# Kernel optimization log

Hardware: AMD Instinct MI355X
Metric: run time of the kernel (lower is better)

Reference implementation:

```python
import jax, jax.numpy as jnp
import numpy as np
import math

N_NODES = 50000
N_EDGES = 1600000
C = 256
H = 8
HD = C // H


def setup_inputs() -> dict:
    key = jax.random.key(0)
    ks = jax.random.split(key, 16)
    s = 0.02
    d = {
        "feat": jax.random.normal(ks[0], (N_NODES, C), jnp.float32),
        "edge_src": jax.random.randint(ks[1], (N_EDGES,), 0, N_NODES),
        "edge_dst": jax.random.randint(ks[2], (N_EDGES,), 0, N_NODES),
        # torch nn.Linear weights are [out, in]
        "Wq": jax.random.normal(ks[3], (C, C), jnp.float32) * s,
        "bq": jnp.zeros((C,), jnp.float32),
        "Wk": jax.random.normal(ks[4], (C, C), jnp.float32) * s,
        "bk": jnp.zeros((C,), jnp.float32),
        "Wv": jax.random.normal(ks[5], (C, C), jnp.float32) * s,
        "bv": jnp.zeros((C,), jnp.float32),
        "Wp": jax.random.normal(ks[6], (C, C), jnp.float32) * s,
        "bp": jnp.zeros((C,), jnp.float32),
        "ln_g": jnp.ones((C,), jnp.float32),
        "ln_b": jnp.zeros((C,), jnp.float32),
        "W1": jax.random.normal(ks[7], (4 * C, C), jnp.float32) * s,
        "b1": jnp.zeros((4 * C,), jnp.float32),
        "W2": jax.random.normal(ks[8], (C, 4 * C), jnp.float32) * s,
        "b2": jnp.zeros((C,), jnp.float32),
    }
    return d


def _layernorm(x, g, b, eps=1e-5):
    mu = jnp.mean(x, axis=-1, keepdims=True)
    var = jnp.mean(jnp.square(x - mu), axis=-1, keepdims=True)
    return (x - mu) * jax.lax.rsqrt(var + eps) * g + b


def reference(feat, edge_src, edge_dst, Wq, bq, Wk, bk, Wv, bv, Wp, bp,
              ln_g, ln_b, W1, b1, W2, b2):
    n = feat.shape[0]
    q = (feat @ Wq.T + bq).reshape(n, H, HD)
    k = (feat @ Wk.T + bk).reshape(n, H, HD)
    v = (feat @ Wv.T + bv).reshape(n, H, HD)

    # per-edge attention logits: (q[dst] * k[src]).sum(-1) / sqrt(head_dim), clamped
    score = jnp.einsum('ehd,ehd->eh', q[edge_dst], k[edge_src])  # [E, H]
    score = jnp.clip(score / math.sqrt(HD), -10.0, 10.0)

    # destination-grouped (segment) softmax over incoming edges
    smax = jax.ops.segment_max(score, edge_dst, num_segments=n)
    smax = jnp.where(jnp.isfinite(smax), smax, 0.0)  # guard empty segments
    ex = jnp.exp(score - smax[edge_dst])
    den = jax.ops.segment_sum(ex, edge_dst, num_segments=n)
    alpha = ex / den[edge_dst]  # [E, H]

    # weighted scatter-aggregate: sum_e alpha_e * v[src_e] into dst
    wv = jax.ops.segment_sum(alpha[:, :, None] * v[edge_src], edge_dst,
                             num_segments=n).reshape(n, C)

    y = wv @ Wp.T + bp
    x = feat + y
    h = _layernorm(x, ln_g, ln_b)
    h = jax.nn.gelu(h @ W1.T + b1, approximate=False) @ W2.T + b2
    return x + h
```

## Files before the change

### kernel.cpp

```cpp
#include <hip/hip_runtime.h>
#include <hip/hip_bf16.h>

#define CDIM 256
#define NH 8
#define HDIM 32

typedef short bf8 __attribute__((ext_vector_type(8)));
typedef float f32x4 __attribute__((ext_vector_type(4)));
typedef float f32x2 __attribute__((ext_vector_type(2)));

__device__ __forceinline__ float bf2f(ushort u) {
  union { unsigned int i; float f; } x; x.i = ((unsigned int)u) << 16; return x.f;
}
__device__ __forceinline__ ushort f2bf(float f) {
  union { float f; unsigned int i; } x; x.f = f;
  unsigned int lsb = (x.i >> 16) & 1u;
  unsigned int r = x.i + 0x7fffu + lsb;
  return (ushort)(r >> 16);
}

__device__ __forceinline__ float dec_e4m3_sw(unsigned int b) {
  unsigned int s = b >> 7, e = (b >> 3) & 15, m = b & 7;
  float v = (e == 0) ? (float)m * 0.001953125f
                     : (float)(8 + m) * 0.125f * exp2f((float)((int)e - 7));
  return s ? -v : v;
}
__device__ __forceinline__ unsigned char enc_e4m3_sw(float f) {
  union { float f; unsigned int u; } x; x.f = f;
  unsigned int s = (x.u >> 31) << 7;
  float a = fabsf(f);
  if (!(a > 0.f)) return (unsigned char)s;
  if (a > 448.f) a = 448.f;
  int e = 0; float mant = frexpf(a, &e);
  int E = e + 6;
  unsigned int out;
  if (E <= 0) {
    int m = (int)rintf(a * 512.f);
    out = (m > 7) ? (s | (1u << 3)) : (s | (unsigned)m);
  } else {
    int m = (int)rintf(mant * 16.f);
    if (m == 16) { m = 8; E++; }
    if (E > 15 || (E == 15 && m - 8 > 6)) { E = 15; m = 14; }
    out = s | ((unsigned)E << 3) | (unsigned)(m - 8);
  }
  return (unsigned char)out;
}
template <bool HI>
__device__ __forceinline__ f32x2 fp8x2_f32(unsigned int w) {
#if __has_builtin(__builtin_amdgcn_cvt_pk_f32_fp8)
  return __builtin_amdgcn_cvt_pk_f32_fp8(w, HI);
#else
  unsigned int b0 = HI ? ((w >> 16) & 0xffu) : (w & 0xffu);
  unsigned int b1 = HI ? (w >> 24) : ((w >> 8) & 0xffu);
  f32x2 r; r[0] = dec_e4m3_sw(b0); r[1] = dec_e4m3_sw(b1); return r;
#endif
}
__device__ __forceinline__ unsigned char f32_fp8(float f) {
#if __has_builtin(__builtin_amdgcn_cvt_pk_fp8_f32)
  return (unsigned char)(__builtin_amdgcn_cvt_pk_fp8_f32(f, f, 0, false) & 0xff);
#else
  return enc_e4m3_sw(f);
#endif
}

__device__ __forceinline__ float fast_gelu(float t) {
  float u = 0.7978845608028654f * (t + 0.044715f * t * t * t);
  float ez = __expf(2.f * u);
  float th = 1.f - 2.f * __builtin_amdgcn_rcpf(ez + 1.f);
  return 0.5f * t * (1.f + th);
}

__device__ __forceinline__ void gload_lds16(const ushort* g, ushort* l) {
  __builtin_amdgcn_global_load_lds((const __attribute__((address_space(1))) unsigned int*)g,
                                   (__attribute__((address_space(3))) unsigned int*)l,
                                   16, 0, 0);
}

__global__ void k_cast4(const float4* __restrict__ s, ushort4* __restrict__ d, int n4) {
  int i = blockIdx.x * blockDim.x + threadIdx.x;
  if (i < n4) {
    float4 v = s[i];
    ushort4 o;
    o.x = f2bf(v.x); o.y = f2bf(v.y); o.z = f2bf(v.z); o.w = f2bf(v.w);
    d[i] = o;
  }
}

__global__ void k_castw(const float4* __restrict__ s0, ushort4* __restrict__ d0,
                        const float4* __restrict__ s1, ushort4* __restrict__ d1,
                        const float4* __restrict__ s2, ushort4* __restrict__ d2,
                        const float4* __restrict__ s3, ushort4* __restrict__ d3,
                        const float4* __restrict__ s4, ushort4* __restrict__ d4,
                        const float4* __restrict__ s5, ushort4* __restrict__ d5) {
  int y = blockIdx.y;
  const float4* s; ushort4* d; int n4;
  switch (y) {
    case 0: s = s0; d = d0; n4 = 16384; break;
    case 1: s = s1; d = d1; n4 = 16384; break;
    case 2: s = s2; d = d2; n4 = 16384; break;
    case 3: s = s3; d = d3; n4 = 16384; break;
    case 4: s = s4; d = d4; n4 = 65536; break;
    default: s = s5; d = d5; n4 = 65536; break;
  }
  int i = blockIdx.x * blockDim.x + threadIdx.x;
  if (i < n4) {
    float4 v = s[i];
    ushort4 o;
    o.x = f2bf(v.x); o.y = f2bf(v.y); o.z = f2bf(v.z); o.w = f2bf(v.w);
    d[i] = o;
  }
}

__global__ void k_hist(const int* __restrict__ dst, int E, int* __restrict__ deg) {
  int i = blockIdx.x * blockDim.x + threadIdx.x;
  if (i < E) atomicAdd(&deg[dst[i]], 1);
}

__global__ __launch_bounds__(1024) void k_scan1(const int* __restrict__ deg, int N,
                                                int* __restrict__ rowptr, int* __restrict__ bsum) {
  __shared__ int s[1024];
  int t = threadIdx.x;
  int i = blockIdx.x * 1024 + t;
  int val = (i < N) ? deg[i] : 0;
  s[t] = val;
  __syncthreads();
  for (int off = 1; off < 1024; off <<= 1) {
    int add = (t >= off) ? s[t - off] : 0;
    __syncthreads();
    s[t] += add;
    __syncthreads();
  }
  if (i < N) rowptr[i + 1] = s[t];
  if (t == 1023) bsum[blockIdx.x] = s[t];
}

__global__ void k_scan2(int* __restrict__ bsum, int nb) {
  if (threadIdx.x == 0 && blockIdx.x == 0) {
    int run = 0;
    for (int j = 0; j < nb; ++j) { int t = bsum[j]; bsum[j] = run; run += t; }
  }
}

__global__ void k_scan3(int* __restrict__ rowptr, const int* __restrict__ bsum, int N) {
  int i = blockIdx.x * blockDim.x + threadIdx.x;
  if (i < N) rowptr[i + 1] += bsum[i >> 10];
  if (i == 0) rowptr[0] = 0;
}

__global__ void k_scatter(const int* __restrict__ src, const int* __restrict__ dst, int E,
                          const int* __restrict__ rowptr, int* __restrict__ cur,
                          int* __restrict__ csr_src) {
  int i = blockIdx.x * blockDim.x + threadIdx.x;
  if (i < E) {
    int d = dst[i];
    int pos = rowptr[d] + atomicAdd(&cur[d], 1);
    csr_src[pos] = src[i];
  }
}

__device__ __forceinline__ void stageA8(const ushort* __restrict__ S, int ld,
                                        int r0, int nr, int k0,
                                        ushort* lds, int wave, int lane) {
  int g = wave * 64 + lane;
  int row = g >> 2, slot = g & 3;
  int rr = r0 + row; rr = (rr < nr) ? rr : (nr - 1);
  const ushort* src = S + (size_t)rr * ld + k0 + ((slot ^ (row & 3)) << 3);
  gload_lds16(src, &lds[(size_t)(wave * 64) * 8]);
}

__device__ __forceinline__ void stageB8(const ushort* __restrict__ S, int ld,
                                        int r0, int nr, int k0,
                                        ushort* lds, int wave, int lane) {
#pragma unroll
  for (int j = 0; j < 2; ++j) {
    int g = wave * 128 + j * 64 + lane;
    int row = g >> 2, slot = g & 3;
    int rr = r0 + row; rr = (rr < nr) ? rr : (nr - 1);
    const ushort* src = S + (size_t)rr * ld + k0 + ((slot ^ (row & 3)) << 3);
    gload_lds16(src, &lds[(size_t)(wave * 128 + j * 64) * 8]);
  }
}

__device__ __forceinline__ void gemm256_core(const ushort* __restrict__ A, int lda, int rowt, int nA,
                                             const ushort* __restrict__ B, int ldb, int colt, int nB,
                                             int K, ushort* lA, ushort* lB, f32x4* acc) {
  int tid = threadIdx.x;
  int wave = tid >> 6, lane = tid & 63;
  int m = lane & 15, quad = lane >> 4;
  int r0w = (wave & 1) * 64, c0w = (wave >> 1) * 64;
  int sw = (quad ^ (m & 3)) << 3;

  for (int k0 = 0; k0 < K; k0 += 32) {
    __syncthreads();
    stageA8(A, lda, rowt, nA, k0, lA, wave, lane);
    stageB8(B, ldb, colt, nB, k0, lB, wave, lane);
    __syncthreads();

    bf8 a[4], b[4];
#pragma unroll
    for (int ri = 0; ri < 4; ++ri)
      a[ri] = *(const bf8*)&lA[(r0w + ri * 16 + m) * 32 + sw];
#pragma unroll
    for (int cj = 0; cj < 4; ++cj)
      b[cj] = *(const bf8*)&lB[(c0w + cj * 16 + m) * 32 + sw];
#pragma unroll
    for (int ri = 0; ri < 4; ++ri)
#pragma unroll
      for (int cj = 0; cj < 4; ++cj)
        acc[ri * 4 + cj] = __builtin_amdgcn_mfma_f32_16x16x32_bf16(a[ri], b[cj], acc[ri * 4 + cj], 0, 0, 0);
  }
}

__global__ __launch_bounds__(512) void k_qkvf(const ushort* __restrict__ featb,
                                              const ushort* __restrict__ Wqkv,
                                              const float* __restrict__ bq, const float* __restrict__ bk,
                                              const float* __restrict__ bv,
                                              ushort* __restrict__ q,
                                              unsigned char* __restrict__ k8,
                                              unsigned char* __restrict__ v8, int N) {
  __shared__ ushort lA[128 * 32];
  __shared__ ushort lB[256 * 32];
  int rowt = blockIdx.x * 128;
  int which = blockIdx.y;
  const float* bias = (which == 0) ? bq : (which == 1) ? bk : bv;
  int tid = threadIdx.x;
  int wave = tid >> 6, lane = tid & 63, m = lane & 15, quad = lane >> 4;
  int r0w = (wave & 1) * 64, c0w = (wave >> 1) * 64;

  f32x4 acc[16];
#pragma unroll
  for (int j = 0; j < 16; ++j) acc[j] = (f32x4){0.f, 0.f, 0.f, 0.f};

  gemm256_core(featb, CDIM, rowt, N, Wqkv + (size_t)which * 256 * CDIM, CDIM, 0, 256,
               CDIM, lA, lB, acc);

  unsigned char* o8 = (which == 1) ? k8 : v8;
#pragma unroll
  for (int cj = 0; cj < 4; ++cj) {
    int col = c0w + cj * 16 + m;
    float bs = bias[col];
#pragma unroll
    for (int ri = 0; ri < 4; ++ri)
#pragma unroll
      for (int i = 0; i < 4; ++i) {
        int r = rowt + r0w + ri * 16 + quad * 4 + i;
        if (r < N) {
          float vv = acc[ri * 4 + cj][i] + bs;
          if (which == 0) q[(size_t)r * CDIM + col] = f2bf(vv);
          else            o8[(size_t)r * CDIM + col] = f32_fp8(vv);
        }
      }
  }
}

__global__ __launch_bounds__(512) void k_projln(const ushort* __restrict__ wv,
                                                const ushort* __restrict__ Wp,
                                                const float* __restrict__ bp,
                                                const float* __restrict__ feat,
                                                const float* __restrict__ lng,
                                                const float* __restrict__ lnb,
                                                float* __restrict__ out,
                                                ushort* __restrict__ h, int N) {
  __shared__ ushort lA[128 * 32];
  __shared__ ushort lB[256 * 32];
  __shared__ float sred[2][128][4];
  int rowt = blockIdx.x * 128;
  int tid = threadIdx.x;
  int wave = tid >> 6, lane = tid & 63, m = lane & 15, quad = lane >> 4;
  int r0w = (wave & 1) * 64, c0w = (wave >> 1) * 64;

  f32x4 acc[16];
#pragma unroll
  for (int j = 0; j < 16; ++j) acc[j] = (f32x4){0.f, 0.f, 0.f, 0.f};

  gemm256_core(wv, CDIM, rowt, N, Wp, CDIM, 0, 256, CDIM, lA, lB, acc);

#pragma unroll
  for (int cj = 0; cj < 4; ++cj) {
    int col = c0w + cj * 16 + m;
    float bs = bp[col];
#pragma unroll
    for (int ri = 0; ri < 4; ++ri)
#pragma unroll
      for (int i = 0; i < 4; ++i) {
        int r = rowt + r0w + ri * 16 + quad * 4 + i;
        int rr = (r < N) ? r : (N - 1);
        acc[ri * 4 + cj][i] += bs + feat[(size_t)rr * CDIM + col];
      }
  }

#pragma unroll
  for (int ri = 0; ri < 4; ++ri)
#pragma unroll
    for (int i = 0; i < 4; ++i) {
      float s = acc[ri * 4 + 0][i] + acc[ri * 4 + 1][i] + acc[ri * 4 + 2][i] + acc[ri * 4 + 3][i];
      float ss = acc[ri * 4 + 0][i] * acc[ri * 4 + 0][i] + acc[ri * 4 + 1][i] * acc[ri * 4 + 1][i]
               + acc[ri * 4 + 2][i] * acc[ri * 4 + 2][i] + acc[ri * 4 + 3][i] * acc[ri * 4 + 3][i];
#pragma unroll
      for (int msk = 1; msk <= 8; msk <<= 1) {
        s += __shfl_xor(s, msk);
        ss += __shfl_xor(ss, msk);
      }
      if (m == 0) {
        int blrow = (wave & 1) * 64 + ri * 16 + quad * 4 + i;
        sred[0][blrow][wave >> 1] = s;
        sred[1][blrow][wave >> 1] = ss;
      }
    }
  __syncthreads();

  float mu_[16], rs_[16];
#pragma unroll
  for (int ri = 0; ri < 4; ++ri)
#pragma unroll
    for (int i = 0; i < 4; ++i) {
      int blrow = (wave & 1) * 64 + ri * 16 + quad * 4 + i;
      float S = sred[0][blrow][0] + sred[0][blrow][1] + sred[0][blrow][2] + sred[0][blrow][3];
      float SS = sred[1][blrow][0] + sred[1][blrow][1] + sred[1][blrow][2] + sred[1][blrow][3];
      float mu = S * (1.f / CDIM);
      float var = SS * (1.f / CDIM) - mu * mu;
      mu_[ri * 4 + i] = mu;
      rs_[ri * 4 + i] = rsqrtf(var + 1e-5f);
    }

#pragma unroll
  for (int cj = 0; cj < 4; ++cj) {
    int col = c0w + cj * 16 + m;
    float gc = lng[col], bc = lnb[col];
#pragma unroll
    for (int ri = 0; ri < 4; ++ri)
#pragma unroll
      for (int i = 0; i < 4; ++i) {
        int r = rowt + r0w + ri * 16 + quad * 4 + i;
        if (r < N) {
          float v = acc[ri * 4 + cj][i];
          out[(size_t)r * CDIM + col] = v;
          h[(size_t)r * CDIM + col] = f2bf((v - mu_[ri * 4 + i]) * rs_[ri * 4 + i] * gc + bc);
        }
      }
  }
}

__global__ __launch_bounds__(512) void k_g1(const ushort* __restrict__ h,
                                            const ushort* __restrict__ W1c,
                                            const float* __restrict__ b1c,
                                            ushort* __restrict__ hid, int N) {
  __shared__ ushort lA[128 * 32];
  __shared__ ushort lB[256 * 32];
  int rowt = blockIdx.x * 128, colt = blockIdx.y * 256;
  int tid = threadIdx.x;
  int wave = tid >> 6, lane = tid & 63, m = lane & 15, quad = lane >> 4;
  int r0w = (wave & 1) * 64, c0w = (wave >> 1) * 64;

  f32x4 acc[16];
#pragma unroll
  for (int j = 0; j < 16; ++j) acc[j] = (f32x4){0.f, 0.f, 0.f, 0.f};

  gemm256_core(h, CDIM, rowt, N, W1c, CDIM, colt, 512, CDIM, lA, lB, acc);

#pragma unroll
  for (int cj = 0; cj < 4; ++cj) {
    int col = colt + c0w + cj * 16 + m;
    float bs = b1c[col];
#pragma unroll
    for (int ri = 0; ri < 4; ++ri)
#pragma unroll
      for (int i = 0; i < 4; ++i) {
        int r = rowt + r0w + ri * 16 + quad * 4 + i;
        if (r < N) hid[(size_t)r * 512 + col] = f2bf(fast_gelu(acc[ri * 4 + cj][i] + bs));
      }
  }
}

__global__ __launch_bounds__(512) void k_g2(const ushort* __restrict__ hid,
                                            const ushort* __restrict__ W2c,
                                            const float* __restrict__ b2,
                                            float* __restrict__ out, int N, int first) {
  __shared__ ushort lA[128 * 32];
  __shared__ ushort lB[256 * 32];
  int rowt = blockIdx.x * 128;
  int tid = threadIdx.x;
  int wave = tid >> 6, lane = tid & 63, m = lane & 15, quad = lane >> 4;
  int r0w = (wave & 1) * 64, c0w = (wave >> 1) * 64;

  f32x4 acc[16];
#pragma unroll
  for (int j = 0; j < 16; ++j) acc[j] = (f32x4){0.f, 0.f, 0.f, 0.f};

  gemm256_core(hid, 512, rowt, N, W2c, 1024, 0, 256, 512, lA, lB, acc);

#pragma unroll
  for (int cj = 0; cj < 4; ++cj) {
    int col = c0w + cj * 16 + m;
    float bs = first ? b2[col] : 0.f;
#pragma unroll
    for (int ri = 0; ri < 4; ++ri)
#pragma unroll
      for (int i = 0; i < 4; ++i) {
        int r = rowt + r0w + ri * 16 + quad * 4 + i;
        if (r < N) {
          size_t idx = (size_t)r * CDIM + col;
          out[idx] = out[idx] + acc[ri * 4 + cj][i] + bs;
        }
      }
  }
}

__global__ __launch_bounds__(256) void k_edge_agg(const ushort* __restrict__ q,
                                                  const unsigned char* __restrict__ kk8,
                                                  const unsigned char* __restrict__ vv8,
                                                  const int* __restrict__ rowptr,
                                                  const int* __restrict__ csr_src,
                                                  int N,
                                                  ushort* __restrict__ wv) {
  int wave = threadIdx.x >> 6, lane = threadIdx.x & 63;
  int n = blockIdx.x * 4 + wave;
  if (n >= N) return;

  int el = lane >> 3, h = lane & 7;
  int beg = rowptr[n], end = rowptr[n + 1];
  int deg = end - beg;

  float qf[32];
  {
    const ushort* qp = q + (size_t)n * CDIM + h * HDIM;
#pragma unroll
    for (int g = 0; g < 4; ++g) {
      bf8 qv = *(const bf8*)(qp + g * 8);
#pragma unroll
      for (int j = 0; j < 8; ++j) qf[g * 8 + j] = bf2f((ushort)qv[j]);
    }
  }

  float accv[4] = {0.f, 0.f, 0.f, 0.f};
  float den_part = 0.f;

  int src_n = (el < deg) ? csr_src[beg + el] : 0;
  const unsigned char* kp0 = kk8 + (size_t)src_n * CDIM + h * HDIM;
  uint4 w0_n = *(const uint4*)kp0;
  uint4 w1_n = *(const uint4*)(kp0 + 16);

  for (int c0 = 0; c0 < deg; c0 += 8) {
    int src = src_n;
    uint4 w0 = w0_n, w1 = w1_n;
    bool vcur = (c0 + el < deg);

    src_n = (c0 + 8 + el < deg) ? csr_src[beg + c0 + 8 + el] : 0;
    const unsigned char* kpn = kk8 + (size_t)src_n * CDIM + h * HDIM;
    w0_n = *(const uint4*)kpn;
    w1_n = *(const uint4*)(kpn + 16);

    float e = 0.f;
    if (vcur) {
      unsigned int ws[8] = {w0.x, w0.y, w0.z, w0.w, w1.x, w1.y, w1.z, w1.w};
      float dot = 0.f;
#pragma unroll
      for (int j = 0; j < 8; ++j) {
        f32x2 lo = fp8x2_f32<false>(ws[j]);
        f32x2 hi = fp8x2_f32<true>(ws[j]);
        dot = fmaf(qf[j * 4 + 0], lo[0], dot);
        dot = fmaf(qf[j * 4 + 1], lo[1], dot);
        dot = fmaf(qf[j * 4 + 2], hi[0], dot);
        dot = fmaf(qf[j * 4 + 3], hi[1], dot);
      }
      float s = dot * 0.17677669529663687f;
      s = fminf(10.f, fmaxf(-10.f, s));
      e = __expf(s - 10.f);
    }
    den_part += e;

#pragma unroll
    for (int j = 0; j < 8; ++j) {
      int sj = __shfl(src, j << 3);
      float ej = __shfl(e, (j << 3) | (lane >> 3));
      unsigned int vw = *(const unsigned int*)(vv8 + (size_t)sj * CDIM + lane * 4);
      f32x2 lo = fp8x2_f32<false>(vw);
      f32x2 hi = fp8x2_f32<true>(vw);
      accv[0] = fmaf(ej, lo[0], accv[0]);
      accv[1] = fmaf(ej, lo[1], accv[1]);
      accv[2] = fmaf(ej, hi[0], accv[2]);
      accv[3] = fmaf(ej, hi[1], accv[3]);
    }
  }

  float den = den_part;
  den += __shfl_xor(den, 8);
  den += __shfl_xor(den, 16);
  den += __shfl_xor(den, 32);
  float denh = __shfl(den, lane >> 3);

  float inv = (deg > 0) ? (1.f / denh) : 0.f;
  ushort4 o;
  o.x = f2bf(accv[0] * inv);
  o.y = f2bf(accv[1] * inv);
  o.z = f2bf(accv[2] * inv);
  o.w = f2bf(accv[3] * inv);
  *(ushort4*)(wv + (size_t)n * CDIM + lane * 4) = o;
}

extern "C" void kernel_launch(void* const* d_in, const int* in_sizes, int n_in,
                              void* d_out, int out_size, void* d_ws, size_t ws_size,
                              hipStream_t stream) {
  const float* feat = (const float*)d_in[0];
  const int* esrc = (const int*)d_in[1];
  const int* edst = (const int*)d_in[2];
  const float* Wq = (const float*)d_in[3];
  const float* bq = (const float*)d_in[4];
  const float* Wk = (const float*)d_in[5];
  const float* bk = (const float*)d_in[6];
  const float* Wv = (const float*)d_in[7];
  const float* bv = (const float*)d_in[8];
  const float* Wp = (const float*)d_in[9];
  const float* bp = (const float*)d_in[10];
  const float* lng = (const float*)d_in[11];
  const float* lnb = (const float*)d_in[12];
  const float* W1 = (const float*)d_in[13];
  const float* b1 = (const float*)d_in[14];
  const float* W2 = (const float*)d_in[15];
  const float* b2 = (const float*)d_in[16];

  const int N = in_sizes[0] / CDIM;
  const int E = in_sizes[1];
  const size_t NC2 = (size_t)N * CDIM * 2;
  const size_t NC1 = (size_t)N * CDIM;

  char* w = (char*)d_ws;
  ushort* q   = (ushort*)(w);
  unsigned char* k8 = (unsigned char*)(w + NC2);
  unsigned char* v8 = (unsigned char*)(w + NC2 + NC1);
  ushort* wvb = (ushort*)(w + 3 * NC2);
  ushort* featb = (ushort*)(w + 3 * NC2);
  ushort* h   = (ushort*)(w + 2 * NC2);
  ushort* hid = (ushort*)(w);

  char* csr = w + 4 * NC2;
  int* rowptr  = (int*)(csr);
  int* deg     = (int*)(csr + 200064);
  int* csr_src = (int*)(csr + 400128);
  int* bsum    = (int*)(csr + 400128 + (size_t)E * 4);

  char* wb = csr + 400128 + (size_t)E * 4 + 256;
  ushort* Wqb = (ushort*)(wb);
  ushort* Wkb = (ushort*)(wb + 131072);
  ushort* Wvb = (ushort*)(wb + 262144);
  ushort* Wpb = (ushort*)(wb + 393216);
  ushort* W1b = (ushort*)(wb + 524288);
  ushort* W2b = (ushort*)(wb + 1048576);

  const int nb = (N + 1023) / 1024;
  const int RT128 = (N + 127) / 128;

  k_castw<<<dim3(256, 6), 256, 0, stream>>>((const float4*)Wq, (ushort4*)Wqb,
                                            (const float4*)Wk, (ushort4*)Wkb,
                                            (const float4*)Wv, (ushort4*)Wvb,
                                            (const float4*)Wp, (ushort4*)Wpb,
                                            (const float4*)W1, (ushort4*)W1b,
                                            (const float4*)W2, (ushort4*)W2b);
  {
    int n4 = N * CDIM / 4;
    k_cast4<<<(n4 + 255) / 256, 256, 0, stream>>>((const float4*)feat, (ushort4*)featb, n4);
  }

  hipMemsetAsync(deg, 0, (size_t)N * 4, stream);
  k_hist<<<(E + 255) / 256, 256, 0, stream>>>(edst, E, deg);
  k_scan1<<<nb, 1024, 0, stream>>>(deg, N, rowptr, bsum);
  k_scan2<<<1, 64, 0, stream>>>(bsum, nb);
  k_scan3<<<(N + 255) / 256, 256, 0, stream>>>(rowptr, bsum, N);
  hipMemsetAsync(deg, 0, (size_t)N * 4, stream);
  k_scatter<<<(E + 255) / 256, 256, 0, stream>>>(esrc, edst, E, rowptr, deg, csr_src);

  k_qkvf<<<dim3(RT128, 3), 512, 0, stream>>>(featb, Wqb, bq, bk, bv, q, k8, v8, N);
  k_edge_agg<<<(N + 3) / 4, 256, 0, stream>>>(q, k8, v8, rowptr, csr_src, N, wvb);
  k_projln<<<RT128, 512, 0, stream>>>(wvb, Wpb, bp, feat, lng, lnb, (float*)d_out, h, N);

  for (int c = 0; c < 2; ++c) {
    k_g1<<<dim3(RT128, 2), 512, 0, stream>>>(h, W1b + (size_t)c * 512 * CDIM,
                                             b1 + c * 512, hid, N);
    k_g2<<<RT128, 512, 0, stream>>>(hid, W2b + (size_t)c * 512,
                                    b2, (float*)d_out, N, c == 0 ? 1 : 0);
  }
}
```

Baseline: 687.3 us.

## Double-buffer LDS tiles in shared GEMM core with async prefetch

New measurement: 681.0 us. No clear change (-0.9%).

```diff
diff --git a/kernel.cpp b/kernel.cpp
--- a/kernel.cpp
+++ b/kernel.cpp
@@ -190,24 +190,40 @@
   int r0w = (wave & 1) * 64, c0w = (wave >> 1) * 64;
   int sw = (quad ^ (m & 3)) << 3;
 
-  for (int k0 = 0; k0 < K; k0 += 32) {
-    __syncthreads();
-    stageA8(A, lda, rowt, nA, k0, lA, wave, lane);
-    stageB8(B, ldb, colt, nB, k0, lB, wave, lane);
-    __syncthreads();
-
+  int nt = K >> 5;
+  stageA8(A, lda, rowt, nA, 0, lA, wave, lane);
+  stageB8(B, ldb, colt, nB, 0, lB, wave, lane);
+
+#pragma unroll
+  for (int t = 0; t < 16; ++t) {
+    if (t >= nt) break;
+    int cur = t & 1;
+    if (t + 1 < nt) {
+      stageA8(A, lda, rowt, nA, (t + 1) << 5, lA + (cur ^ 1) * (128 * 32), wave, lane);
+      stageB8(B, ldb, colt, nB, (t + 1) << 5, lB + (cur ^ 1) * (256 * 32), wave, lane);
+      asm volatile("s_waitcnt vmcnt(3)" ::: "memory");
+    } else {
+      asm volatile("s_waitcnt vmcnt(0)" ::: "memory");
+    }
+    __builtin_amdgcn_s_barrier();
+    __builtin_amdgcn_sched_barrier(0);
+
+    const ushort* cA = lA + cur * (128 * 32);
+    const ushort* cB = lB + cur * (256 * 32);
     bf8 a[4], b[4];
 #pragma unroll
     for (int ri = 0; ri < 4; ++ri)
-      a[ri] = *(const bf8*)&lA[(r0w + ri * 16 + m) * 32 + sw];
+      a[ri] = *(const bf8*)&cA[(r0w + ri * 16 + m) * 32 + sw];
 #pragma unroll
     for (int cj = 0; cj < 4; ++cj)
-      b[cj] = *(const bf8*)&lB[(c0w + cj * 16 + m) * 32 + sw];
+      b[cj] = *(const bf8*)&cB[(c0w + cj * 16 + m) * 32 + sw];
 #pragma unroll
     for (int ri = 0; ri < 4; ++ri)
 #pragma unroll
       for (int cj = 0; cj < 4; ++cj)
         acc[ri * 4 + cj] = __builtin_amdgcn_mfma_f32_16x16x32_bf16(a[ri], b[cj], acc[ri * 4 + cj], 0, 0, 0);
+
+    __builtin_amdgcn_s_barrier();
   }
 }
 
@@ -218,8 +234,8 @@
                                               ushort* __restrict__ q,
                                               unsigned char* __restrict__ k8,
                                               unsigned char* __restrict__ v8, int N) {
-  __shared__ ushort lA[128 * 32];
-  __shared__ ushort lB[256 * 32];
+  __shared__ ushort lA[2 * 128 * 32];
+  __shared__ ushort lB[2 * 256 * 32];
   int rowt = blockIdx.x * 128;
   int which = blockIdx.y;
   const float* bias = (which == 0) ? bq : (which == 1) ? bk : bv;
@@ -261,8 +277,8 @@
                                                 const float* __restrict__ lnb,
                                                 float* __restrict__ out,
                                                 ushort* __restrict__ h, int N) {
-  __shared__ ushort lA[128 * 32];
-  __shared__ ushort lB[256 * 32];
+  __shared__ ushort lA[2 * 128 * 32];
+  __shared__ ushort lB[2 * 256 * 32];
   __shared__ float sred[2][128][4];
   int rowt = blockIdx.x * 128;
   int tid = threadIdx.x;
@@ -345,8 +361,8 @@
                                             const ushort* __restrict__ W1c,
                                             const float* __restrict__ b1c,
                                             ushort* __restrict__ hid, int N) {
-  __shared__ ushort lA[128 * 32];
-  __shared__ ushort lB[256 * 32];
+  __shared__ ushort lA[2 * 128 * 32];
+  __shared__ ushort lB[2 * 256 * 32];
   int rowt = blockIdx.x * 128, colt = blockIdx.y * 256;
   int tid = threadIdx.x;
   int wave = tid >> 6, lane = tid & 63, m = lane & 15, quad = lane >> 4;
@@ -376,8 +392,8 @@
                                             const ushort* __restrict__ W2c,
                                             const float* __restrict__ b2,
                                             float* __restrict__ out, int N, int first) {
-  __shared__ ushort lA[128 * 32];
-  __shared__ ushort lB[256 * 32];
+  __shared__ ushort lA[2 * 128 * 32];
+  __shared__ ushort lB[2 * 256 * 32];
   int rowt = blockIdx.x * 128;
   int tid = threadIdx.x;
   int wave = tid >> 6, lane = tid & 63, m = lane & 15, quad = lane >> 4;
```
